# Performance work log

Measured on AMD Instinct MI355X. Metric: run time of the kernel, lower is better.

The kernel has to match this reference:

```python
import jax, jax.numpy as jnp
import numpy as np

N, E = 16384, 262144
NS_N, NV_N = 128, 64      # node irreps: 128x0e + 64x1o
NS_E, NV_E = 64, 32       # edge irreps: 64x0e + 32x1o
C_OH, LAT = 16, 128
DS, DV = 128, 64          # irreps_out: 128x0e + 64x1o
GS = DS + DV              # gate input scalars (128 act scalars + 64 gates)
SC = 2 * NS_N + NS_E      # 320 concatenated scalar channels
VC = 2 * NV_N + NV_E      # 160 concatenated l=1 channels
M0_IN = SC + VC           # 480 m=0 features into SO2 linear
M0_OUT = GS + DV          # 256 m=0 outputs
AVG_NEI = 16.0
EPS = 1e-8


def setup_inputs() -> dict:
    key = jax.random.key(0)
    ks = jax.random.split(key, 20)
    f = lambda k, s: jax.random.normal(k, s, dtype=jnp.float32)
    return dict(
        node_feat=f(ks[0], (N, NS_N + 3 * NV_N)),
        edge_feat=f(ks[1], (E, NS_E + 3 * NV_E)),
        edge_vec=f(ks[2], (E, 3)),
        latents=f(ks[3], (E, LAT)),
        node_onehot=jax.nn.one_hot(jax.random.randint(ks[4], (N,), 0, C_OH), C_OH, dtype=jnp.float32),
        ln_n_g0=jnp.ones(NS_N), ln_n_b0=jnp.zeros(NS_N), ln_n_g1=jnp.ones(NV_N),
        ln_e_g0=jnp.ones(NS_E), ln_e_b0=jnp.zeros(NS_E), ln_e_g1=jnp.ones(NV_E),
        W_m0=f(ks[5], (M0_IN, M0_OUT)),
        w_r=f(ks[6], (VC, DV)), w_i=f(ks[7], (VC, DV)),
        W_env=f(ks[8], (LAT, DS + DV)),
        Wp0=f(ks[9], (DS, DS)), bp0=jnp.zeros(DS), Wpv=f(ks[10], (DV, DV)),
        Wtp0=f(ks[11], (DS, C_OH, GS)), Wtp1=f(ks[12], (DV, C_OH, DV)),
        Wo0=f(ks[13], (DS, DS)), bo0=jnp.zeros(DS), Wov=f(ks[14], (DV, DV)),
        res_param=jnp.zeros(()),
        edge_index=jax.random.randint(ks[15], (2, E), 0, N),
    )


def _sep_ln(s, v, g0, b0, g1):
    # separable equivariant layer norm: LN on scalars, per-sample RMS on l=1 block
    mu = s.mean(-1, keepdims=True)
    var = jnp.mean((s - mu) ** 2, -1, keepdims=True)
    s = (s - mu) * jax.lax.rsqrt(var + EPS) * g0 + b0
    vvar = jnp.mean(v * v, axis=(-2, -1), keepdims=True)  # component norm, degree-balanced (single l=1)
    v = v * jax.lax.rsqrt(vvar + EPS) * g1[None, :, None]
    return s, v


def _edge_frame(vec):
    # orthonormal frame (a, e1, e2) with a along the edge
    a = vec * jax.lax.rsqrt(jnp.sum(vec * vec, -1, keepdims=True) + EPS)
    helper = jnp.where(jnp.abs(a[:, 2:3]) < 0.99,
                       jnp.array([0.0, 0.0, 1.0], dtype=vec.dtype),
                       jnp.array([1.0, 0.0, 0.0], dtype=vec.dtype))
    e1 = jnp.cross(helper, a)
    e1 = e1 * jax.lax.rsqrt(jnp.sum(e1 * e1, -1, keepdims=True) + EPS)
    e2 = jnp.cross(a, e1)
    return a, e1, e2


def reference(node_feat, edge_feat, edge_vec, latents, node_onehot,
              ln_n_g0, ln_n_b0, ln_n_g1, ln_e_g0, ln_e_b0, ln_e_g1,
              W_m0, w_r, w_i, W_env, Wp0, bp0, Wpv,
              Wtp0, Wtp1, Wo0, bo0, Wov, res_param, edge_index):
    src, dst = edge_index[0], edge_index[1]
    ns, nv = node_feat[:, :NS_N], node_feat[:, NS_N:].reshape(-1, NV_N, 3)
    es, ev = edge_feat[:, :NS_E], edge_feat[:, NS_E:].reshape(-1, NV_E, 3)
    ns, nv = _sep_ln(ns, nv, ln_n_g0, ln_n_b0, ln_n_g1)
    es, ev = _sep_ln(es, ev, ln_e_g0, ln_e_b0, ln_e_g1)
    # per-edge concat: node[src] + edge + node[dst]
    s_cat = jnp.concatenate([ns[src], es, ns[dst]], -1)          # [E, SC]
    v_cat = jnp.concatenate([nv[src], ev, nv[dst]], 1)           # [E, VC, 3]
    # SO2 linear: rotate into edge frame, mix per |m|, rotate back
    a, e1, e2 = _edge_frame(edge_vec)
    c0 = jnp.einsum('eci,ei->ec', v_cat, a)
    c1 = jnp.einsum('eci,ei->ec', v_cat, e1)
    c2 = jnp.einsum('eci,ei->ec', v_cat, e2)
    m0 = jnp.concatenate([s_cat, c0], -1) @ W_m0 * (1.0 / np.sqrt(M0_IN))  # [E, M0_OUT]
    s_out, c0o = m0[:, :GS], m0[:, GS:]
    inv = 1.0 / np.sqrt(VC)
    c1o = (c1 @ w_r - c2 @ w_i) * inv
    c2o = (c1 @ w_i + c2 @ w_r) * inv
    v_out = (c0o[..., None] * a[:, None, :] + c1o[..., None] * e1[:, None, :]
             + c2o[..., None] * e2[:, None, :])                  # [E, DV, 3]
    # gate activation
    s_act = jax.nn.silu(s_out[:, :DS])
    gates = jax.nn.sigmoid(s_out[:, DS:])
    v_g = v_out * gates[..., None]
    # lin_post (per-l linear, scalar bias)
    s2 = s_act @ Wp0 * (1.0 / np.sqrt(DS)) + bp0
    v2 = jnp.einsum('eui,uv->evi', v_g, Wpv) * (1.0 / np.sqrt(DV))
    # env weighting from latents (E3ElementLinear, per-irrep-channel scalars)
    w = latents @ W_env * (1.0 / np.sqrt(LAT))
    s2 = s2 * w[:, :DS]
    v2 = v2 * w[:, DS:, None]
    nrm = 1.0 / np.sqrt(AVG_NEI)
    sa = jax.ops.segment_sum(s2, dst, num_segments=N) * nrm
    va = jax.ops.segment_sum(v2, dst, num_segments=N) * nrm
    # one-hot FullyConnectedTensorProduct (in2 all 0e) + gate + linear
    t0 = jnp.einsum('nu,nc,ucv->nv', sa, node_onehot, Wtp0) * (1.0 / np.sqrt(DS * C_OH))
    t1 = jnp.einsum('nui,nc,ucv->nvi', va, node_onehot, Wtp1) * (1.0 / np.sqrt(DV * C_OH))
    s3 = jax.nn.silu(t0[:, :DS])
    v3 = t1 * jax.nn.sigmoid(t0[:, DS:])[..., None]
    s4 = s3 @ Wo0 * (1.0 / np.sqrt(DS)) + bo0
    v4 = jnp.einsum('nui,uv->nvi', v3, Wov) * (1.0 / np.sqrt(DV))
    new = jnp.concatenate([s4, v4.reshape(-1, 3 * DV)], -1)
    r = jax.nn.sigmoid(res_param)
    return r * node_feat + (1.0 - r) * new
```

## Files before the change

kernel.cpp:

```cpp
#include <hip/hip_runtime.h>
#include <math.h>

#define N_NODES 16384
#define N_EDGES 262144
#define EPSF 1e-8f

#define OFF_X     0
#define OFF_C12   31232
#define OFF_LAT   52224
#define OFF_FR    60928
#define OFF_EDST  62464
#define OFF_WENV  62592
#define POOL_BYTES 75392
#define OFF_SACT  0
#define OFF_GATE  8704
#define OFF_C0O   17408
#define OFF_C1O   31232
#define OFF_C2O   39936
#define OFF_VG    8704

typedef __bf16 bf16x8 __attribute__((ext_vector_type(8)));
typedef float  f32x4  __attribute__((ext_vector_type(4)));

__device__ __forceinline__ f32x4 MFMA16(bf16x8 a, bf16x8 b, f32x4 c){
  return __builtin_amdgcn_mfma_f32_16x16x32_bf16(a, b, c, 0, 0, 0);
}

__device__ __forceinline__ unsigned short f2bf(float x){
  union { float f; unsigned u; } c; c.f = x;
  unsigned u = c.u;
  u += 0x7FFFu + ((u>>16)&1u);
  return (unsigned short)(u>>16);
}
__device__ __forceinline__ float bf2f(unsigned short h){
  union { unsigned u; float f; } c; c.u = ((unsigned)h)<<16;
  return c.f;
}
__device__ __forceinline__ float wsum64(float v){
  #pragma unroll
  for (int m=1; m<64; m<<=1) v += __shfl_xor(v, m);
  return v;
}
__device__ __forceinline__ float wsum32(float v){
  #pragma unroll
  for (int m=1; m<32; m<<=1) v += __shfl_xor(v, m);
  return v;
}
__device__ __forceinline__ float sigm(float x){ return 1.0f/(1.0f+__expf(-x)); }
__device__ __forceinline__ float silu(float x){ return x/(1.0f+__expf(-x)); }

__global__ __launch_bounds__(256) void k_pack(const float* __restrict__ src,
                                              unsigned short* __restrict__ dst,
                                              int K, int N){
  int i = blockIdx.x*256 + threadIdx.x;
  if (i >= K*N) return;
  int k = i / N, n = i - k*N;
  int idx = (((k>>5)*N + n)*4 + ((k>>3)&3))*8 + (k&7);
  dst[idx] = f2bf(src[i]);
}
__global__ __launch_bounds__(256) void k_pack_wc(const float* __restrict__ wr,
                                                 const float* __restrict__ wi,
                                                 unsigned short* __restrict__ dst){
  int i = blockIdx.x*256 + threadIdx.x;
  if (i >= 320*128) return;
  int k = i >> 7, n = i & 127;
  float v;
  if (k < 160) v = (n < 64) ? wr[k*64 + n]        : wi[k*64 + (n-64)];
  else         v = (n < 64) ? -wi[(k-160)*64 + n] : wr[(k-160)*64 + (n-64)];
  int idx = (((k>>5)*128 + n)*4 + ((k>>3)&3))*8 + (k&7);
  dst[idx] = f2bf(v);
}

__global__ __launch_bounds__(256) void k_hist(const int* __restrict__ eidx, int* __restrict__ cnt){
  int e = blockIdx.x*256 + threadIdx.x;
  if (e < N_EDGES) atomicAdd(&cnt[eidx[N_EDGES+e]], 1);
}
__global__ __launch_bounds__(256) void k_scan(const int* __restrict__ cnt,
                                              int* __restrict__ rowp, int* __restrict__ cursor){
  __shared__ int part[256];
  __shared__ int pref[257];
  const int t = threadIdx.x;
  const int base = t*64;
  int s = 0;
  for (int i=0;i<64;i++) s += cnt[base+i];
  part[t] = s; __syncthreads();
  if (t==0){ int a=0; for (int i=0;i<256;i++){ pref[i]=a; a+=part[i]; } pref[256]=a; }
  __syncthreads();
  int a = pref[t];
  for (int i=0;i<64;i++){ rowp[base+i]=a; cursor[base+i]=a; a += cnt[base+i]; }
  if (t==0) rowp[N_NODES] = pref[256];
}
__global__ __launch_bounds__(256) void k_fill(const int* __restrict__ eidx,
                                              int* __restrict__ cursor, int* __restrict__ perm){
  int e = blockIdx.x*256 + threadIdx.x;
  if (e < N_EDGES){
    int pos = atomicAdd(&cursor[eidx[N_EDGES+e]], 1);
    perm[pos] = e;
  }
}

__global__ __launch_bounds__(256) void k_node_ln(
    const float* __restrict__ nf, const float* __restrict__ g0,
    const float* __restrict__ b0, const float* __restrict__ g1,
    float* __restrict__ ns_ln, float* __restrict__ nv_ln)
{
  const int tid  = threadIdx.x;
  const int lane = tid & 63;
  const int n    = blockIdx.x*4 + (tid>>6);
  const float* row = nf + (size_t)n*320;

  float s0 = row[lane], s1 = row[64+lane];
  float mu = wsum64(s0+s1) * (1.0f/128.0f);
  float d0 = s0-mu, d1 = s1-mu;
  float var = wsum64(d0*d0+d1*d1) * (1.0f/128.0f);
  float rs = rsqrtf(var + EPSF);
  ns_ln[(size_t)n*128 + lane]      = d0*rs*g0[lane]    + b0[lane];
  ns_ln[(size_t)n*128 + 64+lane]   = d1*rs*g0[64+lane] + b0[64+lane];

  float px = row[128+lane*3+0], py = row[128+lane*3+1], pz = row[128+lane*3+2];
  float vvar = wsum64(px*px+py*py+pz*pz) * (1.0f/192.0f);
  float vsc = rsqrtf(vvar + EPSF) * g1[lane];
  nv_ln[(size_t)n*192 + lane*3+0] = px*vsc;
  nv_ln[(size_t)n*192 + lane*3+1] = py*vsc;
  nv_ln[(size_t)n*192 + lane*3+2] = pz*vsc;
}

__global__ __launch_bounds__(256,2) void k_edge(
  const float* __restrict__ ef, const float* __restrict__ evec,
  const float* __restrict__ lats,
  const float* __restrict__ g0e, const float* __restrict__ b0e, const float* __restrict__ g1e,
  const unsigned short* __restrict__ pWm0, const unsigned short* __restrict__ pWc,
  const unsigned short* __restrict__ pWenv, const unsigned short* __restrict__ pWp0,
  const unsigned short* __restrict__ pWpv,
  const float* __restrict__ bp0,
  const int* __restrict__ eidx,
  const float* __restrict__ ns_ln, const float* __restrict__ nv_ln,
  float* __restrict__ sa, float* __restrict__ va,
  _Float16* __restrict__ msg, int use_msg)
{
  extern __shared__ unsigned char pool[];
  const int tid = threadIdx.x;
  unsigned short* Xs   = (unsigned short*)(pool + OFF_X);
  unsigned short* C12s = (unsigned short*)(pool + OFF_C12);
  unsigned short* LTs  = (unsigned short*)(pool + OFF_LAT);
  float* FRf = (float*)(pool + OFF_FR);
  int*   EDST = (int*)(pool + OFF_EDST);
  unsigned short* WEs = (unsigned short*)(pool + OFF_WENV);

  {
    const int ln = tid & 31;
    for (int eo=0; eo<4; ++eo){
      const int el = eo*8 + (tid>>5);
      const size_t ge = (size_t)blockIdx.x*32 + el;
      const int src = eidx[ge];
      const int dst = eidx[N_EDGES + ge];

      float vx=evec[ge*3+0], vy=evec[ge*3+1], vz=evec[ge*3+2];
      float rn = rsqrtf(vx*vx+vy*vy+vz*vz+EPSF);
      float ax=vx*rn, ay=vy*rn, az=vz*rn;
      float hx, hz;
      if (fabsf(az) < 0.99f){ hx=0.f; hz=1.f; } else { hx=1.f; hz=0.f; }
      float e1x = -hz*ay;
      float e1y = hz*ax - hx*az;
      float e1z = hx*ay;
      float rn1 = rsqrtf(e1x*e1x+e1y*e1y+e1z*e1z+EPSF);
      e1x*=rn1; e1y*=rn1; e1z*=rn1;
      float e2x = ay*e1z - az*e1y;
      float e2y = az*e1x - ax*e1z;
      float e2z = ax*e1y - ay*e1x;
      if (ln==0){
        FRf[el*12+0]=ax;  FRf[el*12+1]=ay;  FRf[el*12+2]=az;
        FRf[el*12+3]=e1x; FRf[el*12+4]=e1y; FRf[el*12+5]=e1z;
        FRf[el*12+6]=e2x; FRf[el*12+7]=e2y; FRf[el*12+8]=e2z;
        EDST[el]=dst;
      }

      const float* erow = ef + ge*160;
      float s0=erow[ln], s1=erow[32+ln];
      float mu = wsum32(s0+s1)*(1.f/64.f);
      float d0=s0-mu, d1=s1-mu;
      float var = wsum32(d0*d0+d1*d1)*(1.f/64.f);
      float rs = rsqrtf(var+EPSF);
      Xs[el*488 + 128+ln] = f2bf(d0*rs*g0e[ln]    + b0e[ln]);
      Xs[el*488 + 160+ln] = f2bf(d1*rs*g0e[32+ln] + b0e[32+ln]);

      float wx=erow[64+ln*3+0], wy=erow[64+ln*3+1], wz=erow[64+ln*3+2];
      float vvar = wsum32(wx*wx+wy*wy+wz*wz)*(1.f/96.f);
      float vsc = rsqrtf(vvar+EPSF)*g1e[ln];
      wx*=vsc; wy*=vsc; wz*=vsc;
      Xs  [el*488 + 320+64+ln]   = f2bf(wx*ax +wy*ay +wz*az);
      C12s[el*328 + 64+ln]       = f2bf(wx*e1x+wy*e1y+wz*e1z);
      C12s[el*328 + 160+64+ln]   = f2bf(wx*e2x+wy*e2y+wz*e2z);

      const float* nss = ns_ln + (size_t)src*128;
      const float* nsd = ns_ln + (size_t)dst*128;
      #pragma unroll
      for (int q=0;q<4;q++){
        int idx=ln+32*q;
        Xs[el*488 + idx]     = f2bf(nss[idx]);
        Xs[el*488 + 192+idx] = f2bf(nsd[idx]);
      }

      const float* nvs = nv_ln + (size_t)src*192;
      const float* nvd = nv_ln + (size_t)dst*192;
      #pragma unroll
      for (int q=0;q<2;q++){
        int u = ln+32*q;
        float px=nvs[u*3+0], py=nvs[u*3+1], pz=nvs[u*3+2];
        Xs  [el*488 + 320+u]     = f2bf(px*ax +py*ay +pz*az);
        C12s[el*328 + u]         = f2bf(px*e1x+py*e1y+pz*e1z);
        C12s[el*328 + 160+u]     = f2bf(px*e2x+py*e2y+pz*e2z);
        px=nvd[u*3+0]; py=nvd[u*3+1]; pz=nvd[u*3+2];
        Xs  [el*488 + 320+96+u]  = f2bf(px*ax +py*ay +pz*az);
        C12s[el*328 + 96+u]      = f2bf(px*e1x+py*e1y+pz*e1z);
        C12s[el*328 + 160+96+u]  = f2bf(px*e2x+py*e2y+pz*e2z);
      }

      #pragma unroll
      for (int q=0;q<4;q++){ int k=ln+32*q; LTs[el*136+k] = f2bf(lats[ge*128+k]); }
    }
  }
  __syncthreads();

  const int wid = tid>>6, l = tid&63;
  const int r15 = l&15, g = l>>4;
  const f32x4 zero4 = {0.f,0.f,0.f,0.f};

  f32x4 acc1[2][4], acc2[2][2], acc3[2][3];
  #pragma unroll
  for (int m=0;m<2;m++){
    #pragma unroll
    for (int n=0;n<4;n++) acc1[m][n]=zero4;
    #pragma unroll
    for (int n=0;n<2;n++) acc2[m][n]=zero4;
    #pragma unroll
    for (int n=0;n<3;n++) acc3[m][n]=zero4;
  }

  for (int kc=0;kc<15;kc++){
    bf16x8 a0 = *(const bf16x8*)&Xs[(    r15)*488 + kc*32 + g*8];
    bf16x8 a1 = *(const bf16x8*)&Xs[(16+ r15)*488 + kc*32 + g*8];
    const unsigned short* bp = pWm0 + ((size_t)(kc*256 + wid*64 + r15)*4 + g)*8;
    #pragma unroll
    for (int n=0;n<4;n++){
      bf16x8 b = *(const bf16x8*)(bp + n*512);
      acc1[0][n] = MFMA16(a0,b,acc1[0][n]);
      acc1[1][n] = MFMA16(a1,b,acc1[1][n]);
    }
  }
  for (int kc=0;kc<10;kc++){
    bf16x8 a0 = *(const bf16x8*)&C12s[(    r15)*328 + kc*32 + g*8];
    bf16x8 a1 = *(const bf16x8*)&C12s[(16+ r15)*328 + kc*32 + g*8];
    const unsigned short* bp = pWc + ((size_t)(kc*128 + wid*32 + r15)*4 + g)*8;
    #pragma unroll
    for (int n=0;n<2;n++){
      bf16x8 b = *(const bf16x8*)(bp + n*512);
      acc2[0][n] = MFMA16(a0,b,acc2[0][n]);
      acc2[1][n] = MFMA16(a1,b,acc2[1][n]);
    }
  }
  for (int kc=0;kc<4;kc++){
    bf16x8 a0 = *(const bf16x8*)&LTs[(    r15)*136 + kc*32 + g*8];
    bf16x8 a1 = *(const bf16x8*)&LTs[(16+ r15)*136 + kc*32 + g*8];
    const unsigned short* bp = pWenv + ((size_t)(kc*192 + wid*48 + r15)*4 + g)*8;
    #pragma unroll
    for (int n=0;n<3;n++){
      bf16x8 b = *(const bf16x8*)(bp + n*512);
      acc3[0][n] = MFMA16(a0,b,acc3[0][n]);
      acc3[1][n] = MFMA16(a1,b,acc3[1][n]);
    }
  }

  #pragma unroll
  for (int m=0;m<2;m++)
    #pragma unroll
    for (int n=0;n<3;n++)
      #pragma unroll
      for (int r=0;r<4;r++){
        int e = m*16 + g*4 + r;
        int j = wid*48 + n*16 + r15;
        WEs[e*200 + j] = f2bf(acc3[m][n][r]*0.08838834764831845f);
      }

  __syncthreads();

  {
    unsigned short* SAs = (unsigned short*)(pool + OFF_SACT);
    float* GAf = (float*)(pool + OFF_GATE);
    float* C0f = (float*)(pool + OFF_C0O);
    #pragma unroll
    for (int m=0;m<2;m++)
      #pragma unroll
      for (int n=0;n<4;n++)
        #pragma unroll
        for (int r=0;r<4;r++){
          int e = m*16 + g*4 + r;
          int j = wid*64 + n*16 + r15;
          float v = acc1[m][n][r]*0.04564354645876384f;
          if (j < 128)      SAs[e*136 + j] = f2bf(silu(v));
          else if (j < 192) GAf[e*68 + (j-128)] = sigm(v);
          else              C0f[e*68 + (j-192)] = v;
        }
    float* C1f = (float*)(pool + OFF_C1O);
    float* C2f = (float*)(pool + OFF_C2O);
    #pragma unroll
    for (int m=0;m<2;m++)
      #pragma unroll
      for (int n=0;n<2;n++)
        #pragma unroll
        for (int r=0;r<4;r++){
          int e = m*16 + g*4 + r;
          int j = wid*32 + n*16 + r15;
          float v = acc2[m][n][r]*0.07905694150420949f;
          if (j < 64) C1f[e*68 + j] = v;
          else        C2f[e*68 + (j-64)] = v;
        }
  }
  __syncthreads();

  {
    const int e = tid>>3, u0 = (tid&7)*8;
    const float* GAf = (const float*)(pool + OFF_GATE);
    const float* C0f = (const float*)(pool + OFF_C0O);
    const float* C1f = (const float*)(pool + OFF_C1O);
    const float* C2f = (const float*)(pool + OFF_C2O);
    float ax=FRf[e*12+0],  ay=FRf[e*12+1],  az=FRf[e*12+2];
    float b1x=FRf[e*12+3], b1y=FRf[e*12+4], b1z=FRf[e*12+5];
    float b2x=FRf[e*12+6], b2y=FRf[e*12+7], b2z=FRf[e*12+8];
    float vgx[8], vgy[8], vgz[8];
    #pragma unroll
    for (int i=0;i<8;i++){
      int u = u0+i;
      float gt = GAf[e*68+u];
      float c0 = C0f[e*68+u], c1 = C1f[e*68+u], c2 = C2f[e*68+u];
      vgx[i] = (c0*ax + c1*b1x + c2*b2x)*gt;
      vgy[i] = (c0*ay + c1*b1y + c2*b2y)*gt;
      vgz[i] = (c0*az + c1*b1z + c2*b2z)*gt;
    }
    __syncthreads();
    unsigned short* VGs = (unsigned short*)(pool + OFF_VG);
    #pragma unroll
    for (int i=0;i<8;i++){
      VGs[0*2304 + e*72 + u0+i] = f2bf(vgx[i]);
      VGs[1*2304 + e*72 + u0+i] = f2bf(vgy[i]);
      VGs[2*2304 + e*72 + u0+i] = f2bf(vgz[i]);
    }
  }
  __syncthreads();

  {
    const unsigned short* SAs = (const unsigned short*)(pool + OFF_SACT);
    const unsigned short* VGs = (const unsigned short*)(pool + OFF_VG);
    f32x4 acc4[2][2], acc5[3][2];
    #pragma unroll
    for (int m=0;m<2;m++){ acc4[m][0]=zero4; acc4[m][1]=zero4; }
    #pragma unroll
    for (int c=0;c<3;c++){ acc5[c][0]=zero4; acc5[c][1]=zero4; }

    for (int kc=0;kc<4;kc++){
      bf16x8 a0 = *(const bf16x8*)&SAs[(    r15)*136 + kc*32 + g*8];
      bf16x8 a1 = *(const bf16x8*)&SAs[(16+ r15)*136 + kc*32 + g*8];
      const unsigned short* bp = pWp0 + ((size_t)(kc*128 + wid*32 + r15)*4 + g)*8;
      #pragma unroll
      for (int n=0;n<2;n++){
        bf16x8 b = *(const bf16x8*)(bp + n*512);
        acc4[0][n] = MFMA16(a0,b,acc4[0][n]);
        acc4[1][n] = MFMA16(a1,b,acc4[1][n]);
      }
    }
    #pragma unroll
    for (int c=0;c<3;c++){
      #pragma unroll
      for (int kc=0;kc<2;kc++){
        bf16x8 a0 = *(const bf16x8*)&VGs[c*2304 + (    r15)*72 + kc*32 + g*8];
        bf16x8 a1 = *(const bf16x8*)&VGs[c*2304 + (16+ r15)*72 + kc*32 + g*8];
        bf16x8 b  = *(const bf16x8*)(pWpv + ((size_t)(kc*64 + wid*16 + r15)*4 + g)*8);
        acc5[c][0] = MFMA16(a0,b,acc5[c][0]);
        acc5[c][1] = MFMA16(a1,b,acc5[c][1]);
      }
    }

    if (use_msg){
      const size_t gebase = (size_t)blockIdx.x*32;
      #pragma unroll
      for (int m=0;m<2;m++)
        #pragma unroll
        for (int n=0;n<2;n++)
          #pragma unroll
          for (int r=0;r<4;r++){
            int e = m*16 + g*4 + r;
            int j = wid*32 + n*16 + r15;
            float v = acc4[m][n][r]*0.08838834764831845f + bp0[j];
            v *= bf2f(WEs[e*200 + j]);
            msg[(gebase+e)*320 + j] = (_Float16)v;
          }
      #pragma unroll
      for (int c=0;c<3;c++)
        #pragma unroll
        for (int m=0;m<2;m++)
          #pragma unroll
          for (int r=0;r<4;r++){
            int e = m*16 + g*4 + r;
            int vch = wid*16 + r15;
            float val = acc5[c][m][r]*0.125f * bf2f(WEs[e*200 + 128 + vch]);
            msg[(gebase+e)*320 + 128 + c*64 + vch] = (_Float16)val;
          }
    } else {
      #pragma unroll
      for (int m=0;m<2;m++)
        #pragma unroll
        for (int n=0;n<2;n++)
          #pragma unroll
          for (int r=0;r<4;r++){
            int e = m*16 + g*4 + r;
            int j = wid*32 + n*16 + r15;
            float v = acc4[m][n][r]*0.08838834764831845f + bp0[j];
            v *= bf2f(WEs[e*200 + j]);
            atomicAdd(&sa[(size_t)EDST[e]*128 + j], v);
          }
      #pragma unroll
      for (int c=0;c<3;c++)
        #pragma unroll
        for (int m=0;m<2;m++)
          #pragma unroll
          for (int r=0;r<4;r++){
            int e = m*16 + g*4 + r;
            int vch = wid*16 + r15;
            float val = acc5[c][m][r]*0.125f * bf2f(WEs[e*200 + 128 + vch]);
            atomicAdd(&va[(size_t)EDST[e]*192 + vch*3 + c], val);
          }
    }
  }
}

__global__ __launch_bounds__(256) void k_node_out(
  const float* __restrict__ nf, const float* __restrict__ oh,
  const float* __restrict__ Wtp0, const float* __restrict__ Wtp1,
  const float* __restrict__ Wo0, const float* __restrict__ bo0,
  const float* __restrict__ Wov, const float* __restrict__ resp,
  const float* __restrict__ sa, const float* __restrict__ va,
  const _Float16* __restrict__ msg, const int* __restrict__ rowp,
  const int* __restrict__ perm, int use_msg,
  float* __restrict__ out)
{
  __shared__ float SAB[4][128];
  __shared__ float VX[4][64], VY[4][64], VZ[4][64];
  __shared__ float S3 [4][128];
  __shared__ float V3 [4][256];
  const int tid=threadIdx.x, lane=tid&63, g=tid>>6;
  const int n = blockIdx.x*4 + g;

  float cf=0.f;
  #pragma unroll
  for (int j=0;j<16;j++) cf += j*oh[(size_t)n*16+j];
  const int c = (int)(cf+0.5f);

  if (use_msg){
    float a0=0.f,a1=0.f,vx=0.f,vy=0.f,vz=0.f;
    const int beg = rowp[n], end = rowp[n+1];
    for (int i=beg;i<end;++i){
      const _Float16* mr = msg + (size_t)perm[i]*320;
      a0 += (float)mr[lane];
      a1 += (float)mr[64+lane];
      vx += (float)mr[128+lane];
      vy += (float)mr[192+lane];
      vz += (float)mr[256+lane];
    }
    SAB[g][lane]    = a0*0.25f;
    SAB[g][64+lane] = a1*0.25f;
    VX[g][lane]=vx*0.25f; VY[g][lane]=vy*0.25f; VZ[g][lane]=vz*0.25f;
  } else {
    SAB[g][lane]    = sa[(size_t)n*128+lane]   *0.25f;
    SAB[g][64+lane] = sa[(size_t)n*128+64+lane]*0.25f;
    VX[g][lane] = va[(size_t)n*192+lane*3+0]*0.25f;
    VY[g][lane] = va[(size_t)n*192+lane*3+1]*0.25f;
    VZ[g][lane] = va[(size_t)n*192+lane*3+2]*0.25f;
  }
  __syncthreads();

  float t00=0.f, t01=0.f, t02=0.f;
  const float* w0c = Wtp0 + (size_t)c*192;
  for (int u=0;u<128;u++){
    float s = SAB[g][u];
    t00 += s * w0c[(size_t)u*3072 + lane];
    t01 += s * w0c[(size_t)u*3072 + lane+64];
    t02 += s * w0c[(size_t)u*3072 + lane+128];
  }
  const float sct0 = 0.02209708691f;
  t00*=sct0; t01*=sct0; t02*=sct0;

  float t1x=0.f,t1y=0.f,t1z=0.f;
  const float* w1c = Wtp1 + (size_t)c*64;
  for (int u=0;u<64;u++){
    float wv = w1c[(size_t)u*1024 + lane];
    t1x += VX[g][u]*wv;
    t1y += VY[g][u]*wv;
    t1z += VZ[g][u]*wv;
  }
  t1x*=0.03125f; t1y*=0.03125f; t1z*=0.03125f;

  S3[g][lane]    = silu(t00);
  S3[g][64+lane] = silu(t01);
  float g2 = sigm(t02);
  float4 v3v = {t1x*g2, t1y*g2, t1z*g2, 0.f};
  *(float4*)&V3[g][lane*4] = v3v;
  __syncthreads();

  float s40=0.f, s41=0.f;
  for (int k=0;k<128;k++){
    float s3k = S3[g][k];
    s40 += s3k*Wo0[k*128+lane];
    s41 += s3k*Wo0[k*128+64+lane];
  }
  s40 = s40*0.08838834765f + bo0[lane];
  s41 = s41*0.08838834765f + bo0[64+lane];

  float v4x=0.f,v4y=0.f,v4z=0.f;
  for (int u=0;u<64;u++){
    float4 v3u = *(const float4*)&V3[g][u*4];
    float wv = Wov[u*64+lane];
    v4x += v3u.x*wv; v4y += v3u.y*wv; v4z += v3u.z*wv;
  }
  v4x*=0.125f; v4y*=0.125f; v4z*=0.125f;

  const float r = sigm(resp[0]);
  const float* row = nf + (size_t)n*320;
  float* orow = out + (size_t)n*320;
  orow[lane]      = r*row[lane]      + (1.f-r)*s40;
  orow[64+lane]   = r*row[64+lane]   + (1.f-r)*s41;
  orow[128+lane*3+0] = r*row[128+lane*3+0] + (1.f-r)*v4x;
  orow[128+lane*3+1] = r*row[128+lane*3+1] + (1.f-r)*v4y;
  orow[128+lane*3+2] = r*row[128+lane*3+2] + (1.f-r)*v4z;
}

extern "C" void kernel_launch(void* const* d_in, const int* in_sizes, int n_in,
                              void* d_out, int out_size, void* d_ws, size_t ws_size,
                              hipStream_t stream)
{
  const float* nf   = (const float*)d_in[0];
  const float* ef   = (const float*)d_in[1];
  const float* evec = (const float*)d_in[2];
  const float* lats = (const float*)d_in[3];
  const float* oh   = (const float*)d_in[4];
  const float* g0n  = (const float*)d_in[5];
  const float* b0n  = (const float*)d_in[6];
  const float* g1n  = (const float*)d_in[7];
  const float* g0e  = (const float*)d_in[8];
  const float* b0e  = (const float*)d_in[9];
  const float* g1e  = (const float*)d_in[10];
  const float* Wm0  = (const float*)d_in[11];
  const float* wr   = (const float*)d_in[12];
  const float* wi   = (const float*)d_in[13];
  const float* Wenv = (const float*)d_in[14];
  const float* Wp0  = (const float*)d_in[15];
  const float* bp0  = (const float*)d_in[16];
  const float* Wpv  = (const float*)d_in[17];
  const float* Wtp0 = (const float*)d_in[18];
  const float* Wtp1 = (const float*)d_in[19];
  const float* Wo0  = (const float*)d_in[20];
  const float* bo0  = (const float*)d_in[21];
  const float* Wov  = (const float*)d_in[22];
  const float* resp = (const float*)d_in[23];
  const int*   eidx = (const int*)d_in[24];

  float* ws    = (float*)d_ws;
  float* ns_ln = ws;
  float* nv_ln = ws + (size_t)N_NODES*128;
  float* sa    = ws + (size_t)N_NODES*320;
  float* va    = ws + (size_t)N_NODES*448;
  unsigned short* wpk = (unsigned short*)(ws + (size_t)N_NODES*640);
  unsigned short* pWm0  = wpk;
  unsigned short* pWc   = wpk + 122880;
  unsigned short* pWenv = wpk + 163840;
  unsigned short* pWp0  = wpk + 188416;
  unsigned short* pWpv  = wpk + 204800;
  int* ibuf   = (int*)(ws + (size_t)N_NODES*640 + 104448);
  int* cnt    = ibuf;
  int* rowp   = ibuf + 16384;
  int* cursor = ibuf + 32769;
  int* perm   = ibuf + 49153;
  _Float16* msg = (_Float16*)(ws + (size_t)N_NODES*640 + 104448 + 311304);

  const size_t need = ((size_t)N_NODES*640 + 104448 + 311304)*4 + (size_t)N_EDGES*320*2;
  const int use_msg = (ws_size >= need) ? 1 : 0;

  k_pack<<<(122880+255)/256, 256, 0, stream>>>(Wm0,  pWm0, 480, 256);
  k_pack_wc<<<(40960+255)/256, 256, 0, stream>>>(wr, wi, pWc);
  k_pack<<<(24576+255)/256, 256, 0, stream>>>(Wenv, pWenv, 128, 192);
  k_pack<<<(16384+255)/256, 256, 0, stream>>>(Wp0,  pWp0, 128, 128);
  k_pack<<<(4096+255)/256,  256, 0, stream>>>(Wpv,  pWpv, 64, 64);
  k_node_ln<<<N_NODES/4, 256, 0, stream>>>(nf, g0n, b0n, g1n, ns_ln, nv_ln);

  if (use_msg){
    hipMemsetAsync(cnt, 0, N_NODES*sizeof(int), stream);
    k_hist<<<(N_EDGES+255)/256, 256, 0, stream>>>(eidx, cnt);
    k_scan<<<1, 256, 0, stream>>>(cnt, rowp, cursor);
    k_fill<<<(N_EDGES+255)/256, 256, 0, stream>>>(eidx, cursor, perm);
  } else {
    hipMemsetAsync(sa, 0, (size_t)N_NODES*320*sizeof(float), stream);
  }

  k_edge<<<N_EDGES/32, 256, POOL_BYTES, stream>>>(ef, evec, lats, g0e, b0e, g1e,
                                                  pWm0, pWc, pWenv, pWp0, pWpv, bp0,
                                                  eidx, ns_ln, nv_ln, sa, va, msg, use_msg);
  k_node_out<<<N_NODES/4, 256, 0, stream>>>(nf, oh, Wtp0, Wtp1, Wo0, bo0, Wov,
                                            resp, sa, va, msg, rowp, perm, use_msg,
                                            (float*)d_out);
}
```

Before: 681.5 us.

## Halve edge tile to 16 and write messages in destination-sorted order

The edge kernel now handles 16 edges per block instead of 32. LDS per block is halved and the launch bound moves to 4 blocks per CU, so more blocks can be resident at once. Edges are read through the dst-sorted permutation, so messages are written in CSR order and the node kernel reads them contiguously without the perm indirection. The cost is that each weight-fragment load now feeds half as many MFMAs, which doubles weight traffic per edge, and the input gathers of edge features and latents become scattered.

Result: slower. 710.5 us (+4.3%).

```diff
diff --git a/kernel.cpp b/kernel.cpp
--- a/kernel.cpp
+++ b/kernel.cpp
@@ -6,18 +6,18 @@
 #define EPSF 1e-8f
 
 #define OFF_X     0
-#define OFF_C12   31232
-#define OFF_LAT   52224
-#define OFF_FR    60928
-#define OFF_EDST  62464
-#define OFF_WENV  62592
-#define POOL_BYTES 75392
+#define OFF_C12   15616
+#define OFF_LAT   26112
+#define OFF_FR    30464
+#define OFF_EDST  31232
+#define OFF_WENV  31296
+#define POOL_BYTES 37696
 #define OFF_SACT  0
-#define OFF_GATE  8704
-#define OFF_C0O   17408
-#define OFF_C1O   31232
-#define OFF_C2O   39936
-#define OFF_VG    8704
+#define OFF_GATE  4352
+#define OFF_C0O   8704
+#define OFF_C1O   15616
+#define OFF_C2O   19968
+#define OFF_VG    4352
 
 typedef __bf16 bf16x8 __attribute__((ext_vector_type(8)));
 typedef float  f32x4  __attribute__((ext_vector_type(4)));
@@ -125,7 +125,7 @@
   nv_ln[(size_t)n*192 + lane*3+2] = pz*vsc;
 }
 
-__global__ __launch_bounds__(256,2) void k_edge(
+__global__ __launch_bounds__(256,4) void k_edge(
   const float* __restrict__ ef, const float* __restrict__ evec,
   const float* __restrict__ lats,
   const float* __restrict__ g0e, const float* __restrict__ b0e, const float* __restrict__ g1e,
@@ -134,6 +134,7 @@
   const unsigned short* __restrict__ pWpv,
   const float* __restrict__ bp0,
   const int* __restrict__ eidx,
+  const int* __restrict__ perm,
   const float* __restrict__ ns_ln, const float* __restrict__ nv_ln,
   float* __restrict__ sa, float* __restrict__ va,
   _Float16* __restrict__ msg, int use_msg)
@@ -149,13 +150,15 @@
 
   {
     const int ln = tid & 31;
-    for (int eo=0; eo<4; ++eo){
+    #pragma unroll
+    for (int eo=0; eo<2; ++eo){
       const int el = eo*8 + (tid>>5);
-      const size_t ge = (size_t)blockIdx.x*32 + el;
-      const int src = eidx[ge];
-      const int dst = eidx[N_EDGES + ge];
-
-      float vx=evec[ge*3+0], vy=evec[ge*3+1], vz=evec[ge*3+2];
+      const int slot = blockIdx.x*16 + el;
+      const size_t e = use_msg ? (size_t)perm[slot] : (size_t)slot;
+      const int src = eidx[e];
+      const int dst = eidx[N_EDGES + e];
+
+      float vx=evec[e*3+0], vy=evec[e*3+1], vz=evec[e*3+2];
       float rn = rsqrtf(vx*vx+vy*vy+vz*vz+EPSF);
       float ax=vx*rn, ay=vy*rn, az=vz*rn;
       float hx, hz;
@@ -175,7 +178,7 @@
         EDST[el]=dst;
       }
 
-      const float* erow = ef + ge*160;
+      const float* erow = ef + e*160;
       float s0=erow[ln], s1=erow[32+ln];
       float mu = wsum32(s0+s1)*(1.f/64.f);
       float d0=s0-mu, d1=s1-mu;
@@ -217,7 +220,7 @@
       }
 
       #pragma unroll
-      for (int q=0;q<4;q++){ int k=ln+32*q; LTs[el*136+k] = f2bf(lats[ge*128+k]); }
+      for (int q=0;q<4;q++){ int k=ln+32*q; LTs[el*136+k] = f2bf(lats[e*128+k]); }
     }
   }
   __syncthreads();
@@ -226,61 +229,50 @@
   const int r15 = l&15, g = l>>4;
   const f32x4 zero4 = {0.f,0.f,0.f,0.f};
 
-  f32x4 acc1[2][4], acc2[2][2], acc3[2][3];
-  #pragma unroll
-  for (int m=0;m<2;m++){
-    #pragma unroll
-    for (int n=0;n<4;n++) acc1[m][n]=zero4;
-    #pragma unroll
-    for (int n=0;n<2;n++) acc2[m][n]=zero4;
-    #pragma unroll
-    for (int n=0;n<3;n++) acc3[m][n]=zero4;
-  }
+  f32x4 acc1[4], acc2[2], acc3[3];
+  #pragma unroll
+  for (int n=0;n<4;n++) acc1[n]=zero4;
+  #pragma unroll
+  for (int n=0;n<2;n++) acc2[n]=zero4;
+  #pragma unroll
+  for (int n=0;n<3;n++) acc3[n]=zero4;
 
   for (int kc=0;kc<15;kc++){
-    bf16x8 a0 = *(const bf16x8*)&Xs[(    r15)*488 + kc*32 + g*8];
-    bf16x8 a1 = *(const bf16x8*)&Xs[(16+ r15)*488 + kc*32 + g*8];
+    bf16x8 a0 = *(const bf16x8*)&Xs[r15*488 + kc*32 + g*8];
     const unsigned short* bp = pWm0 + ((size_t)(kc*256 + wid*64 + r15)*4 + g)*8;
     #pragma unroll
     for (int n=0;n<4;n++){
       bf16x8 b = *(const bf16x8*)(bp + n*512);
-      acc1[0][n] = MFMA16(a0,b,acc1[0][n]);
-      acc1[1][n] = MFMA16(a1,b,acc1[1][n]);
+      acc1[n] = MFMA16(a0,b,acc1[n]);
     }
   }
   for (int kc=0;kc<10;kc++){
-    bf16x8 a0 = *(const bf16x8*)&C12s[(    r15)*328 + kc*32 + g*8];
-    bf16x8 a1 = *(const bf16x8*)&C12s[(16+ r15)*328 + kc*32 + g*8];
+    bf16x8 a0 = *(const bf16x8*)&C12s[r15*328 + kc*32 + g*8];
     const unsigned short* bp = pWc + ((size_t)(kc*128 + wid*32 + r15)*4 + g)*8;
     #pragma unroll
     for (int n=0;n<2;n++){
       bf16x8 b = *(const bf16x8*)(bp + n*512);
-      acc2[0][n] = MFMA16(a0,b,acc2[0][n]);
-      acc2[1][n] = MFMA16(a1,b,acc2[1][n]);
+      acc2[n] = MFMA16(a0,b,acc2[n]);
     }
   }
   for (int kc=0;kc<4;kc++){
-    bf16x8 a0 = *(const bf16x8*)&LTs[(    r15)*136 + kc*32 + g*8];
-    bf16x8 a1 = *(const bf16x8*)&LTs[(16+ r15)*136 + kc*32 + g*8];
+    bf16x8 a0 = *(const bf16x8*)&LTs[r15*136 + kc*32 + g*8];
     const unsigned short* bp = pWenv + ((size_t)(kc*192 + wid*48 + r15)*4 + g)*8;
     #pragma unroll
     for (int n=0;n<3;n++){
       bf16x8 b = *(const bf16x8*)(bp + n*512);
-      acc3[0][n] = MFMA16(a0,b,acc3[0][n]);
-      acc3[1][n] = MFMA16(a1,b,acc3[1][n]);
-    }
-  }
-
-  #pragma unroll
-  for (int m=0;m<2;m++)
-    #pragma unroll
-    for (int n=0;n<3;n++)
-      #pragma unroll
-      for (int r=0;r<4;r++){
-        int e = m*16 + g*4 + r;
-        int j = wid*48 + n*16 + r15;
-        WEs[e*200 + j] = f2bf(acc3[m][n][r]*0.08838834764831845f);
-      }
+      acc3[n] = MFMA16(a0,b,acc3[n]);
+    }
+  }
+
+  #pragma unroll
+  for (int n=0;n<3;n++)
+    #pragma unroll
+    for (int r=0;r<4;r++){
+      int e = g*4 + r;
+      int j = wid*48 + n*16 + r15;
+      WEs[e*200 + j] = f2bf(acc3[n][r]*0.08838834764831845f);
+    }
 
   __syncthreads();
 
@@ -289,37 +281,33 @@
     float* GAf = (float*)(pool + OFF_GATE);
     float* C0f = (float*)(pool + OFF_C0O);
     #pragma unroll
-    for (int m=0;m<2;m++)
-      #pragma unroll
-      for (int n=0;n<4;n++)
-        #pragma unroll
-        for (int r=0;r<4;r++){
-          int e = m*16 + g*4 + r;
-          int j = wid*64 + n*16 + r15;
-          float v = acc1[m][n][r]*0.04564354645876384f;
-          if (j < 128)      SAs[e*136 + j] = f2bf(silu(v));
-          else if (j < 192) GAf[e*68 + (j-128)] = sigm(v);
-          else              C0f[e*68 + (j-192)] = v;
-        }
+    for (int n=0;n<4;n++)
+      #pragma unroll
+      for (int r=0;r<4;r++){
+        int e = g*4 + r;
+        int j = wid*64 + n*16 + r15;
+        float v = acc1[n][r]*0.04564354645876384f;
+        if (j < 128)      SAs[e*136 + j] = f2bf(silu(v));
+        else if (j < 192) GAf[e*68 + (j-128)] = sigm(v);
+        else              C0f[e*68 + (j-192)] = v;
+      }
     float* C1f = (float*)(pool + OFF_C1O);
     float* C2f = (float*)(pool + OFF_C2O);
     #pragma unroll
-    for (int m=0;m<2;m++)
-      #pragma unroll
-      for (int n=0;n<2;n++)
-        #pragma unroll
-        for (int r=0;r<4;r++){
-          int e = m*16 + g*4 + r;
-          int j = wid*32 + n*16 + r15;
-          float v = acc2[m][n][r]*0.07905694150420949f;
-          if (j < 64) C1f[e*68 + j] = v;
-          else        C2f[e*68 + (j-64)] = v;
-        }
+    for (int n=0;n<2;n++)
+      #pragma unroll
+      for (int r=0;r<4;r++){
+        int e = g*4 + r;
+        int j = wid*32 + n*16 + r15;
+        float v = acc2[n][r]*0.07905694150420949f;
+        if (j < 64) C1f[e*68 + j] = v;
+        else        C2f[e*68 + (j-64)] = v;
+      }
   }
   __syncthreads();
 
   {
-    const int e = tid>>3, u0 = (tid&7)*8;
+    const int e = tid>>4, i0 = (tid&15)*4;
     const float* GAf = (const float*)(pool + OFF_GATE);
     const float* C0f = (const float*)(pool + OFF_C0O);
     const float* C1f = (const float*)(pool + OFF_C1O);
@@ -327,10 +315,10 @@
     float ax=FRf[e*12+0],  ay=FRf[e*12+1],  az=FRf[e*12+2];
     float b1x=FRf[e*12+3], b1y=FRf[e*12+4], b1z=FRf[e*12+5];
     float b2x=FRf[e*12+6], b2y=FRf[e*12+7], b2z=FRf[e*12+8];
-    float vgx[8], vgy[8], vgz[8];
-    #pragma unroll
-    for (int i=0;i<8;i++){
-      int u = u0+i;
+    float vgx[4], vgy[4], vgz[4];
+    #pragma unroll
+    for (int i=0;i<4;i++){
+      int u = i0+i;
       float gt = GAf[e*68+u];
       float c0 = C0f[e*68+u], c1 = C1f[e*68+u], c2 = C2f[e*68+u];
       vgx[i] = (c0*ax + c1*b1x + c2*b2x)*gt;
@@ -340,10 +328,10 @@
     __syncthreads();
     unsigned short* VGs = (unsigned short*)(pool + OFF_VG);
     #pragma unroll
-    for (int i=0;i<8;i++){
-      VGs[0*2304 + e*72 + u0+i] = f2bf(vgx[i]);
-      VGs[1*2304 + e*72 + u0+i] = f2bf(vgy[i]);
-      VGs[2*2304 + e*72 + u0+i] = f2bf(vgz[i]);
+    for (int i=0;i<4;i++){
+      VGs[0*1152 + e*72 + i0+i] = f2bf(vgx[i]);
+      VGs[1*1152 + e*72 + i0+i] = f2bf(vgy[i]);
+      VGs[2*1152 + e*72 + i0+i] = f2bf(vgz[i]);
     }
   }
   __syncthreads();
@@ -351,84 +339,71 @@
   {
     const unsigned short* SAs = (const unsigned short*)(pool + OFF_SACT);
     const unsigned short* VGs = (const unsigned short*)(pool + OFF_VG);
-    f32x4 acc4[2][2], acc5[3][2];
-    #pragma unroll
-    for (int m=0;m<2;m++){ acc4[m][0]=zero4; acc4[m][1]=zero4; }
-    #pragma unroll
-    for (int c=0;c<3;c++){ acc5[c][0]=zero4; acc5[c][1]=zero4; }
+    f32x4 acc4[2], acc5[3];
+    acc4[0]=zero4; acc4[1]=zero4;
+    #pragma unroll
+    for (int c=0;c<3;c++) acc5[c]=zero4;
 
     for (int kc=0;kc<4;kc++){
-      bf16x8 a0 = *(const bf16x8*)&SAs[(    r15)*136 + kc*32 + g*8];
-      bf16x8 a1 = *(const bf16x8*)&SAs[(16+ r15)*136 + kc*32 + g*8];
+      bf16x8 a0 = *(const bf16x8*)&SAs[r15*136 + kc*32 + g*8];
       const unsigned short* bp = pWp0 + ((size_t)(kc*128 + wid*32 + r15)*4 + g)*8;
       #pragma unroll
       for (int n=0;n<2;n++){
         bf16x8 b = *(const bf16x8*)(bp + n*512);
-        acc4[0][n] = MFMA16(a0,b,acc4[0][n]);
-        acc4[1][n] = MFMA16(a1,b,acc4[1][n]);
+        acc4[n] = MFMA16(a0,b,acc4[n]);
       }
     }
     #pragma unroll
     for (int c=0;c<3;c++){
       #pragma unroll
       for (int kc=0;kc<2;kc++){
-        bf16x8 a0 = *(const bf16x8*)&VGs[c*2304 + (    r15)*72 + kc*32 + g*8];
-        bf16x8 a1 = *(const bf16x8*)&VGs[c*2304 + (16+ r15)*72 + kc*32 + g*8];
+        bf16x8 a0 = *(const bf16x8*)&VGs[c*1152 + r15*72 + kc*32 + g*8];
         bf16x8 b  = *(const bf16x8*)(pWpv + ((size_t)(kc*64 + wid*16 + r15)*4 + g)*8);
-        acc5[c][0] = MFMA16(a0,b,acc5[c][0]);
-        acc5[c][1] = MFMA16(a1,b,acc5[c][1]);
+        acc5[c] = MFMA16(a0,b,acc5[c]);
       }
     }
 
     if (use_msg){
-      const size_t gebase = (size_t)blockIdx.x*32;
-      #pragma unroll
-      for (int m=0;m<2;m++)
+      const size_t sbase = (size_t)blockIdx.x*16;
+      #pragma unroll
+      for (int n=0;n<2;n++)
         #pragma unroll
-        for (int n=0;n<2;n++)
-          #pragma unroll
-          for (int r=0;r<4;r++){
-            int e = m*16 + g*4 + r;
-            int j = wid*32 + n*16 + r15;
-            float v = acc4[m][n][r]*0.08838834764831845f + bp0[j];
-            v *= bf2f(WEs[e*200 + j]);
-            msg[(gebase+e)*320 + j] = (_Float16)v;
-          }
+        for (int r=0;r<4;r++){
+          int e = g*4 + r;
+          int j = wid*32 + n*16 + r15;
+          float v = acc4[n][r]*0.08838834764831845f + bp0[j];
+          v *= bf2f(WEs[e*200 + j]);
+          msg[(sbase+e)*320 + j] = (_Float16)v;
+        }
       #pragma unroll
       for (int c=0;c<3;c++)
         #pragma unroll
-        for (int m=0;m<2;m++)
-          #pragma unroll
-          for (int r=0;r<4;r++){
-            int e = m*16 + g*4 + r;
-            int vch = wid*16 + r15;
-            float val = acc5[c][m][r]*0.125f * bf2f(WEs[e*200 + 128 + vch]);
-            msg[(gebase+e)*320 + 128 + c*64 + vch] = (_Float16)val;
-          }
+        for (int r=0;r<4;r++){
+          int e = g*4 + r;
+          int vch = wid*16 + r15;
+          float val = acc5[c][r]*0.125f * bf2f(WEs[e*200 + 128 + vch]);
+          msg[(sbase+e)*320 + 128 + c*64 + vch] = (_Float16)val;
+        }
     } else {
       #pragma unroll
-      for (int m=0;m<2;m++)
+      for (int n=0;n<2;n++)
         #pragma unroll
-        for (int n=0;n<2;n++)
-          #pragma unroll
-          for (int r=0;r<4;r++){
-            int e = m*16 + g*4 + r;
-            int j = wid*32 + n*16 + r15;
-            float v = acc4[m][n][r]*0.08838834764831845f + bp0[j];
-            v *= bf2f(WEs[e*200 + j]);
-            atomicAdd(&sa[(size_t)EDST[e]*128 + j], v);
-          }
+        for (int r=0;r<4;r++){
+          int e = g*4 + r;
+          int j = wid*32 + n*16 + r15;
+          float v = acc4[n][r]*0.08838834764831845f + bp0[j];
+          v *= bf2f(WEs[e*200 + j]);
+          atomicAdd(&sa[(size_t)EDST[e]*128 + j], v);
+        }
       #pragma unroll
       for (int c=0;c<3;c++)
         #pragma unroll
-        for (int m=0;m<2;m++)
-          #pragma unroll
-          for (int r=0;r<4;r++){
-            int e = m*16 + g*4 + r;
-            int vch = wid*16 + r15;
-            float val = acc5[c][m][r]*0.125f * bf2f(WEs[e*200 + 128 + vch]);
-            atomicAdd(&va[(size_t)EDST[e]*192 + vch*3 + c], val);
-          }
+        for (int r=0;r<4;r++){
+          int e = g*4 + r;
+          int vch = wid*16 + r15;
+          float val = acc5[c][r]*0.125f * bf2f(WEs[e*200 + 128 + vch]);
+          atomicAdd(&va[(size_t)EDST[e]*192 + vch*3 + c], val);
+        }
     }
   }
 }
@@ -440,7 +415,7 @@
   const float* __restrict__ Wov, const float* __restrict__ resp,
   const float* __restrict__ sa, const float* __restrict__ va,
   const _Float16* __restrict__ msg, const int* __restrict__ rowp,
-  const int* __restrict__ perm, int use_msg,
+  int use_msg,
   float* __restrict__ out)
 {
   __shared__ float SAB[4][128];
@@ -459,7 +434,7 @@
     float a0=0.f,a1=0.f,vx=0.f,vy=0.f,vz=0.f;
     const int beg = rowp[n], end = rowp[n+1];
     for (int i=beg;i<end;++i){
-      const _Float16* mr = msg + (size_t)perm[i]*320;
+      const _Float16* mr = msg + (size_t)i*320;
       a0 += (float)mr[lane];
       a1 += (float)mr[64+lane];
       vx += (float)mr[128+lane];
@@ -600,10 +575,10 @@
     hipMemsetAsync(sa, 0, (size_t)N_NODES*320*sizeof(float), stream);
   }
 
-  k_edge<<<N_EDGES/32, 256, POOL_BYTES, stream>>>(ef, evec, lats, g0e, b0e, g1e,
+  k_edge<<<N_EDGES/16, 256, POOL_BYTES, stream>>>(ef, evec, lats, g0e, b0e, g1e,
                                                   pWm0, pWc, pWenv, pWp0, pWpv, bp0,
-                                                  eidx, ns_ln, nv_ln, sa, va, msg, use_msg);
+                                                  eidx, perm, ns_ln, nv_ln, sa, va, msg, use_msg);
   k_node_out<<<N_NODES/4, 256, 0, stream>>>(nf, oh, Wtp0, Wtp1, Wo0, bo0, Wov,
-                                            resp, sa, va, msg, rowp, perm, use_msg,
+                                            resp, sa, va, msg, rowp, use_msg,
                                             (float*)d_out);
 }
```
